# Optimization experiments

Hardware: AMD Instinct MI355X
Metric: run time of the kernel (lower is better)

Reference implementation:

```python
import jax, jax.numpy as jnp
import numpy as np

HIDDEN = 128
RHO = 5        # K // 2 with K = 10
J = 5
SCALE = 5.0


def setup_inputs() -> dict:
    key = jax.random.key(0)
    ks = jax.random.split(key, 16)
    B, N, D = 2, 4096, HIDDEN
    eigvs = jax.random.uniform(ks[0], (B, N, D), dtype=jnp.float32)  # eigenvalue encodings in [0,1)
    x = jax.random.normal(ks[1], (B, N, D), dtype=jnp.float32)
    U = jax.random.normal(ks[2], (B, N, N), dtype=jnp.float32) / np.sqrt(N)
    s = 1.0 / np.sqrt(D)
    return {
        "eigvs": eigvs, "x": x, "U": U,
        # Linear weights stored as [in, out] (already transposed vs torch)
        "Wa": jax.random.normal(ks[3], (D, RHO), dtype=jnp.float32) * s,
        "ba": jnp.zeros((RHO,), jnp.float32),
        "Wb": jax.random.normal(ks[4], (D, RHO), dtype=jnp.float32) * s,
        "bb": jnp.zeros((RHO,), jnp.float32),
        "Ws": jax.random.normal(ks[5], (D, J), dtype=jnp.float32) * s,
        "bs": jnp.zeros((J,), jnp.float32),
        "WS": jax.random.normal(ks[6], (D, D), dtype=jnp.float32) * s,
        "bS": jnp.zeros((D,), jnp.float32),
        "WM": jax.random.normal(ks[7], (J, D, D), dtype=jnp.float32) * s,
        "bM": jnp.zeros((J, D), jnp.float32),
        "Ww": jax.random.normal(ks[8], (D, D), dtype=jnp.float32) * s,
        "bw": jnp.zeros((D,), jnp.float32),
    }


def _generate_g(a, sx, rho):
    # a: [B, rho]; sx: [B, J, N, D] scaled eigenvalues. Even Chebyshev polys.
    T_odd = jnp.ones_like(sx)
    T_even = sx
    g = a[:, 0, None, None, None] * T_even
    for i in range(1, rho):
        T_odd = 2.0 * sx * T_even - T_odd
        T_even = 2.0 * sx * T_odd - T_even
        g = g + a[:, i, None, None, None] * T_even
    return g


def _generate_h(b, e, rho):
    # b: [B, rho]; e: [B, N, D]. Odd Chebyshev polys.
    T_odd = jnp.ones_like(e)
    T_even = e
    h = b[:, 0, None, None] * T_odd
    for i in range(1, rho):
        T_odd = 2.0 * e * T_even - T_odd
        T_even = 2.0 * e * T_odd - T_even
        h = h + b[:, i, None, None] * T_odd
    return h


def reference(eigvs, x, U, Wa, ba, Wb, bb, Ws, bs, WS, bS, WM, bM, Ww, bw):
    # Filter coefficients from pooled eigenvalue encodings
    a_tilde = (eigvs @ Wa + ba).mean(axis=-2)                      # [B, rho]
    b_tilde = (eigvs @ Wb + bb).mean(axis=-2)                      # [B, rho]
    scale_tilde = jax.nn.sigmoid((eigvs @ Ws + bs).mean(axis=-2)) * SCALE  # [B, J]

    h = _generate_h(b_tilde, eigvs, RHO)                           # [B, N, D] scaling filter
    sx = scale_tilde[:, :, None, None] * eigvs[:, None]            # [B, J, N, D]
    g = _generate_g(a_tilde, sx, RHO)                              # [B, J, N, D] wavelet filters

    # Spectral convolution: U diag(filter) U^T x, per channel
    xt = jnp.einsum('bmn,bmd->bnd', U, x)                          # U^T x
    y_h = jnp.einsum('bnm,bmd->bnd', U, h * xt)                    # [B, N, D]
    y_g = jnp.einsum('bnm,bjmd->bjnd', U, g * xt[:, None])         # [B, J, N, D]

    out = y_h @ WS + bS                                            # S_kernel
    out = out + jnp.einsum('bjnd,jde->bne', y_g, WM) + bM.sum(0)   # sum_j M_kernels[j]
    return out @ Ww + bw                                           # W
```

## Files before the change

kernel.cpp:

```cpp
#include <hip/hip_runtime.h>
#include <hip/hip_bf16.h>
#include <stdint.h>

typedef unsigned short u16;
typedef __attribute__((ext_vector_type(8))) short bf16x8;
typedef __attribute__((ext_vector_type(4))) float f32x4;
typedef __attribute__((ext_vector_type(4))) uint32_t u32x4;

__device__ inline u16 f2bf(float f) {
  union { float f; uint32_t u; } v; v.f = f;
  uint32_t u = v.u;
  u += 0x7FFFu + ((u >> 16) & 1u);
  return (u16)(u >> 16);
}
__device__ inline uint32_t pkbf(float a, float b) {
  union { __hip_bfloat162 h; uint32_t u; } c;
  c.h = __float22bfloat162_rn(float2{a, b});
  return c.u;
}
__device__ inline float bf2f(u16 h) {
  union { uint32_t u; float f; } v; v.u = (uint32_t)h << 16; return v.f;
}
__device__ inline void gl_lds16(const void* g, void* s) {
  __builtin_amdgcn_global_load_lds(
      (const __attribute__((address_space(1))) void*)(uintptr_t)(g),
      (__attribute__((address_space(3))) void*)(uint32_t)(uintptr_t)(s),
      16, 0, 0);
}

__global__ __launch_bounds__(256) void k_pre(
    const float* __restrict__ eig, const float* __restrict__ x,
    const float* __restrict__ U,
    const float* __restrict__ WS, const float* __restrict__ WM,
    const float* __restrict__ Ww, const float* __restrict__ bS,
    const float* __restrict__ bM, const float* __restrict__ bw,
    float* __restrict__ part, u16* __restrict__ xT,
    u16* __restrict__ VT, float* __restrict__ cvec,
    u16* __restrict__ Ubf, u16* __restrict__ UTr) {
  const int bid = blockIdx.x, t = threadIdx.x;
  __shared__ float red[256];
  __shared__ uint32_t L[64][33];
  if (bid < 64) {
    const int b = bid >> 5, chunk = bid & 31;
    const int d = t & 127, half = t >> 7;
    const float* p = eig + ((long)b * 4096 + chunk * 128 + half) * 128 + d;
    float s = 0.0f;
    for (int i = 0; i < 64; i++) s += p[(long)i * 256];
    red[t] = s;
    __syncthreads();
    if (t < 128) part[((long)b * 32 + chunk) * 128 + d] = red[t] + red[t + 128];
    return;
  }
  if (bid < 320) {
    const int q = bid - 64;
    const int b = q >> 7, rem = q & 127;
    const int tr = rem & 63, tc = rem >> 6;
    const float* I = x + (long)b * 524288;
    u16* O = xT + (long)b * 524288;
    const int r = t >> 2, cq = (t & 3) * 4;
    const float* src = I + (long)(tr * 64 + r) * 128 + tc * 64;
#pragma unroll
    for (int i = 0; i < 4; i++) {
      const float4 f = *(const float4*)(src + cq + 16 * i);
      const int c = cq + 16 * i;
      L[r][(c >> 1)]     = pkbf(f.x, f.y);
      L[r][(c >> 1) + 1] = pkbf(f.z, f.w);
    }
    __syncthreads();
    const int r0 = (t & 7) * 8;
#pragma unroll
    for (int p = 0; p < 2; p++) {
      const int c = (t >> 3) + 32 * p;
      uint32_t w[4];
#pragma unroll
      for (int i = 0; i < 4; i++) {
        const uint32_t w0 = L[r0 + 2 * i][c >> 1];
        const uint32_t w1 = L[r0 + 2 * i + 1][c >> 1];
        const u16 v0 = (c & 1) ? (u16)(w0 >> 16) : (u16)(w0 & 0xffff);
        const u16 v1 = (c & 1) ? (u16)(w1 >> 16) : (u16)(w1 & 0xffff);
        w[i] = (uint32_t)v0 | ((uint32_t)v1 << 16);
      }
      u32x4* dst = (u32x4*)(O + (long)(tc * 64 + c) * 4096 + tr * 64 + r0);
      *dst = u32x4{w[0], w[1], w[2], w[3]};
    }
    return;
  }
  if (bid < 704) {
    const int q = (bid - 320) * 2 + (t >> 7);
    const int e = t & 127;
    const int f = q >> 7, d = q & 127;
    const float* Frow = (f == 0) ? (WS + d * 128) : (WM + ((long)(f - 1) * 128 + d) * 128);
    float s = 0.0f;
    for (int k = 0; k < 128; k++) s += Frow[k] * Ww[k * 128 + e];
    VT[(long)e * 768 + f * 128 + d] = f2bf(s);
    return;
  }
  if (bid == 704) {
    if (t >= 128) return;
    float s = bw[t];
    for (int k = 0; k < 128; k++) {
      float tv = bS[k];
#pragma unroll
      for (int j = 0; j < 5; j++) tv += bM[j * 128 + k];
      s += tv * Ww[k * 128 + t];
    }
    cvec[t] = s;
    return;
  }
  {
    const int q = bid - 705;
    const int b = q >> 12, rem = q & 4095;
    const int ti = rem & 63, tj = rem >> 6;
    const float* Iu = U + (long)b * 16777216 + (long)ti * 64 * 4096 + tj * 64;
    u16* Ou = Ubf + (long)b * 16777216 + (long)ti * 64 * 4096 + tj * 64;
    u16* Ot = UTr + (long)b * 16777216 + (long)tj * 64 * 4096 + ti * 64;
    const int r = t >> 2, cq = (t & 3) * 4;
    const float* src = Iu + (long)r * 4096 + cq;
    u16* dstS = Ou + (long)r * 4096 + cq;
#pragma unroll
    for (int i = 0; i < 4; i++) {
      const float4 f = *(const float4*)(src + 16 * i);
      const int c = cq + 16 * i;
      *(uint2*)(dstS + 16 * i) = uint2{pkbf(f.x, f.y), pkbf(f.z, f.w)};
      L[r][(c >> 1)]     = pkbf(f.x, f.y);
      L[r][(c >> 1) + 1] = pkbf(f.z, f.w);
    }
    __syncthreads();
    const int r0 = (t & 7) * 8;
#pragma unroll
    for (int p = 0; p < 2; p++) {
      const int c = (t >> 3) + 32 * p;
      uint32_t w[4];
#pragma unroll
      for (int i = 0; i < 4; i++) {
        const uint32_t w0 = L[r0 + 2 * i][c >> 1];
        const uint32_t w1 = L[r0 + 2 * i + 1][c >> 1];
        const u16 v0 = (c & 1) ? (u16)(w0 >> 16) : (u16)(w0 & 0xffff);
        const u16 v1 = (c & 1) ? (u16)(w1 >> 16) : (u16)(w1 & 0xffff);
        w[i] = (uint32_t)v0 | ((uint32_t)v1 << 16);
      }
      u32x4* dst = (u32x4*)(Ot + (long)c * 4096 + r0);
      *dst = u32x4{w[0], w[1], w[2], w[3]};
    }
  }
}


__global__ __launch_bounds__(256) void k_gemm1(
    const u16* __restrict__ xT, const u16* __restrict__ UTr,
    const float* __restrict__ part,
    const float* __restrict__ Wa, const float* __restrict__ ba,
    const float* __restrict__ Wb, const float* __restrict__ bb_,
    const float* __restrict__ Ws, const float* __restrict__ bs,
    float* __restrict__ xs, float* __restrict__ coeff) {
  const int tn = blockIdx.x, ks = blockIdx.y, bb = blockIdx.z;
  const int tid = threadIdx.x;
  __shared__ float sd[128];
  __shared__ __align__(16) u16 As[3 * 4096];
  __shared__ __align__(16) u16 Bs[3 * 4096];
  if (tn == 32) {
    if (ks != 0) return;
    if (tid < 128) {
      float s = 0.0f;
      for (int c = 0; c < 32; c++) s += part[((long)bb * 32 + c) * 128 + tid];
      sd[tid] = s * (1.0f / 4096.0f);
    }
    __syncthreads();
    if (tid >= 15) return;
    const int kind = tid / 5, r = tid % 5;
    const float* W = (kind == 0) ? Wa : ((kind == 1) ? Wb : Ws);
    float v = 0.0f;
    for (int d = 0; d < 128; d++) v += sd[d] * W[d * 5 + r];
    v += (kind == 0) ? ba[r] : ((kind == 1) ? bb_[r] : bs[r]);
    if (kind == 2) v = 5.0f / (1.0f + __expf(-v));
    coeff[bb * 16 + kind * 5 + r] = v;
    return;
  }
  const int wave = tid >> 6, lane = tid & 63;
  const int wm = (wave >> 1) * 64, wn = (wave & 1) * 64;
  f32x4 acc[4][4];
#pragma unroll
  for (int i = 0; i < 4; i++)
#pragma unroll
    for (int j = 0; j < 4; j++)
#pragma unroll
      for (int r = 0; r < 4; r++) acc[i][j][r] = 0.0f;
  const int swz_rd = ((lane >> 4) ^ ((lane >> 1) & 3)) * 16;
  const int a_off = (wm + (lane & 15)) * 64 + swz_rd;
  const int b_off = (wn + (lane & 15)) * 64 + swz_rd;
  const int srow = wave * 32 + (lane >> 2);
  const int scol = ((lane & 3) ^ ((lane >> 3) & 3)) * 8;
  const u16* Asrc = xT + (long)bb * 524288 + ks * 512 + scol;
  const u16* Bsrc = UTr + (long)bb * 16777216 + (long)tn * 524288 + ks * 512 + scol;

  auto STAGE = [&](int k0, int buf) {
    char* dA = (char*)As + buf * 8192 + wave * 2048;
    char* dB = (char*)Bs + buf * 8192 + wave * 2048;
    gl_lds16(Asrc + (long)srow * 4096 + k0, dA);
    gl_lds16(Asrc + (long)(srow + 16) * 4096 + k0, dA + 1024);
    gl_lds16(Bsrc + (long)srow * 4096 + k0, dB);
    gl_lds16(Bsrc + (long)(srow + 16) * 4096 + k0, dB + 1024);
  };
  auto COMPUTE = [&](int buf) {
    bf16x8 af[4], bfr[4];
    const char* Ab_ = (const char*)As + buf * 8192 + a_off;
    const char* Bb_ = (const char*)Bs + buf * 8192 + b_off;
#pragma unroll
    for (int mt = 0; mt < 4; mt++) af[mt] = *(const bf16x8*)(Ab_ + mt * 1024);
#pragma unroll
    for (int nt = 0; nt < 4; nt++) bfr[nt] = *(const bf16x8*)(Bb_ + nt * 1024);
#pragma unroll
    for (int mt = 0; mt < 4; mt++)
#pragma unroll
      for (int nt = 0; nt < 4; nt++)
        acc[mt][nt] = __builtin_amdgcn_mfma_f32_16x16x32_bf16(af[mt], bfr[nt], acc[mt][nt], 0, 0, 0);
  };

  STAGE(0, 0);
  STAGE(32, 1);
  asm volatile("s_waitcnt vmcnt(4)" ::: "memory");
  __builtin_amdgcn_s_barrier();
  __builtin_amdgcn_sched_barrier(0);
#pragma unroll
  for (int t = 0; t < 14; ++t) {
    STAGE((t + 2) * 32, (t + 2) % 3);
    COMPUTE(t % 3);
    asm volatile("s_waitcnt vmcnt(4)" ::: "memory");
    __builtin_amdgcn_s_barrier();
    __builtin_amdgcn_sched_barrier(0);
  }
  COMPUTE(2);
  asm volatile("s_waitcnt vmcnt(0)" ::: "memory");
  __builtin_amdgcn_s_barrier();
  __builtin_amdgcn_sched_barrier(0);
  COMPUTE(0);

  const int lr = (lane >> 4) * 4, lc = lane & 15;
  float* Cf = xs + (long)bb * 524288 + (long)ks * 1048576;
#pragma unroll
  for (int mt = 0; mt < 4; mt++)
#pragma unroll
    for (int nt = 0; nt < 4; nt++) {
      const int col = tn * 128 + wn + nt * 16 + lc;
#pragma unroll
      for (int r = 0; r < 4; r++) {
        const int row = wm + mt * 16 + lr + r;
        Cf[(long)col * 128 + row] = acc[mt][nt][r];
      }
    }
}

__global__ void k_filter(const float* __restrict__ eig, const float* __restrict__ xs,
                         const float* __restrict__ coeff, u16* __restrict__ Mod) {
  const int b = blockIdx.y;
  const int n = blockIdx.x * 2 + (threadIdx.x >> 7);
  const int d = threadIdx.x & 127;
  const long ridx = (long)b * 4096 + n;
  const long off = ridx * 128 + d;
  const float e = eig[off];
  float xv = 0.0f;
#pragma unroll
  for (int s = 0; s < 8; s++) xv += xs[off + (long)s * 1048576];
  const float* cf = coeff + b * 16;
  float To = 1.0f, Tev = e;
  float h = cf[5];
#pragma unroll
  for (int i = 1; i < 5; i++) {
    To = 2.0f * e * Tev - To;
    Tev = 2.0f * e * To - Tev;
    h += cf[5 + i] * To;
  }
  u16* row = Mod + ridx * 768;
  row[d] = f2bf(h * xv);
#pragma unroll
  for (int j = 0; j < 5; j++) {
    const float sx = cf[10 + j] * e;
    float To2 = 1.0f, Te2 = sx;
    float g = cf[0] * Te2;
#pragma unroll
    for (int i = 1; i < 5; i++) {
      To2 = 2.0f * sx * Te2 - To2;
      Te2 = 2.0f * sx * To2 - Te2;
      g += cf[i] * Te2;
    }
    row[(j + 1) * 128 + d] = f2bf(g * xv);
  }
}

__global__ __launch_bounds__(256) void k_gemm2(
    const u16* __restrict__ VT, const u16* __restrict__ Mod, u16* __restrict__ wT) {
  const int tn = blockIdx.x, bb = blockIdx.z;
  __shared__ __align__(16) u16 As[3 * 4096];
  __shared__ __align__(16) u16 Bs[3 * 4096];
  const int tid = threadIdx.x, wave = tid >> 6, lane = tid & 63;
  const int wm = (wave >> 1) * 64, wn = (wave & 1) * 64;
  f32x4 acc[4][4];
#pragma unroll
  for (int i = 0; i < 4; i++)
#pragma unroll
    for (int j = 0; j < 4; j++)
#pragma unroll
      for (int r = 0; r < 4; r++) acc[i][j][r] = 0.0f;
  const int swz_rd = ((lane >> 4) ^ ((lane >> 1) & 3)) * 16;
  const int a_off = (wm + (lane & 15)) * 64 + swz_rd;
  const int b_off = (wn + (lane & 15)) * 64 + swz_rd;
  const int srow = wave * 32 + (lane >> 2);
  const int scol = ((lane & 3) ^ ((lane >> 3) & 3)) * 8;
  const u16* Asrc = VT + scol;
  const u16* Bsrc = Mod + (long)bb * 3145728 + (long)tn * 98304 + scol;

  auto STAGE = [&](int k0, int buf) {
    char* dA = (char*)As + buf * 8192 + wave * 2048;
    char* dB = (char*)Bs + buf * 8192 + wave * 2048;
    gl_lds16(Asrc + (long)srow * 768 + k0, dA);
    gl_lds16(Asrc + (long)(srow + 16) * 768 + k0, dA + 1024);
    gl_lds16(Bsrc + (long)srow * 768 + k0, dB);
    gl_lds16(Bsrc + (long)(srow + 16) * 768 + k0, dB + 1024);
  };
  auto COMPUTE = [&](int buf) {
    bf16x8 af[4], bfr[4];
    const char* Ab_ = (const char*)As + buf * 8192 + a_off;
    const char* Bb_ = (const char*)Bs + buf * 8192 + b_off;
#pragma unroll
    for (int mt = 0; mt < 4; mt++) af[mt] = *(const bf16x8*)(Ab_ + mt * 1024);
#pragma unroll
    for (int nt = 0; nt < 4; nt++) bfr[nt] = *(const bf16x8*)(Bb_ + nt * 1024);
#pragma unroll
    for (int mt = 0; mt < 4; mt++)
#pragma unroll
      for (int nt = 0; nt < 4; nt++)
        acc[mt][nt] = __builtin_amdgcn_mfma_f32_16x16x32_bf16(af[mt], bfr[nt], acc[mt][nt], 0, 0, 0);
  };

  STAGE(0, 0);
  STAGE(32, 1);
  asm volatile("s_waitcnt vmcnt(4)" ::: "memory");
  __builtin_amdgcn_s_barrier();
  __builtin_amdgcn_sched_barrier(0);
#pragma unroll
  for (int t = 0; t < 22; ++t) {
    STAGE((t + 2) * 32, (t + 2) % 3);
    COMPUTE(t % 3);
    asm volatile("s_waitcnt vmcnt(4)" ::: "memory");
    __builtin_amdgcn_s_barrier();
    __builtin_amdgcn_sched_barrier(0);
  }
  COMPUTE(1);
  asm volatile("s_waitcnt vmcnt(0)" ::: "memory");
  __builtin_amdgcn_s_barrier();
  __builtin_amdgcn_sched_barrier(0);
  COMPUTE(2);

  const int lr = (lane >> 4) * 4, lc = lane & 15;
  u16* Cb = wT + (long)bb * 524288;
#pragma unroll
  for (int mt = 0; mt < 4; mt++)
#pragma unroll
    for (int nt = 0; nt < 4; nt++) {
      const int col = tn * 128 + wn + nt * 16 + lc;
#pragma unroll
      for (int r = 0; r < 4; r++) {
        const int row = wm + mt * 16 + lr + r;
        Cb[(long)row * 4096 + col] = f2bf(acc[mt][nt][r]);
      }
    }
}

__global__ __launch_bounds__(256) void k_gemm3(
    const u16* __restrict__ Ubf, const u16* __restrict__ wT, u16* __restrict__ os16) {
  const int tm = blockIdx.x, ks = blockIdx.y, bb = blockIdx.z;
  __shared__ __align__(16) u16 As[3 * 4096];
  __shared__ __align__(16) u16 Bs[3 * 4096];
  const int tid = threadIdx.x, wave = tid >> 6, lane = tid & 63;
  const int wm = (wave >> 1) * 64, wn = (wave & 1) * 64;
  f32x4 acc[4][4];
#pragma unroll
  for (int i = 0; i < 4; i++)
#pragma unroll
    for (int j = 0; j < 4; j++)
#pragma unroll
      for (int r = 0; r < 4; r++) acc[i][j][r] = 0.0f;
  const int swz_rd = ((lane >> 4) ^ ((lane >> 1) & 3)) * 16;
  const int a_off = (wm + (lane & 15)) * 64 + swz_rd;
  const int b_off = (wn + (lane & 15)) * 64 + swz_rd;
  const int srow = wave * 32 + (lane >> 2);
  const int scol = ((lane & 3) ^ ((lane >> 3) & 3)) * 8;
  const u16* Asrc = Ubf + (long)bb * 16777216 + (long)tm * 524288 + ks * 512 + scol;
  const u16* Bsrc = wT + (long)bb * 524288 + ks * 512 + scol;

  auto STAGE = [&](int k0, int buf) {
    char* dA = (char*)As + buf * 8192 + wave * 2048;
    char* dB = (char*)Bs + buf * 8192 + wave * 2048;
    gl_lds16(Asrc + (long)srow * 4096 + k0, dA);
    gl_lds16(Asrc + (long)(srow + 16) * 4096 + k0, dA + 1024);
    gl_lds16(Bsrc + (long)srow * 4096 + k0, dB);
    gl_lds16(Bsrc + (long)(srow + 16) * 4096 + k0, dB + 1024);
  };
  auto COMPUTE = [&](int buf) {
    bf16x8 af[4], bfr[4];
    const char* Ab_ = (const char*)As + buf * 8192 + a_off;
    const char* Bb_ = (const char*)Bs + buf * 8192 + b_off;
#pragma unroll
    for (int mt = 0; mt < 4; mt++) af[mt] = *(const bf16x8*)(Ab_ + mt * 1024);
#pragma unroll
    for (int nt = 0; nt < 4; nt++) bfr[nt] = *(const bf16x8*)(Bb_ + nt * 1024);
#pragma unroll
    for (int mt = 0; mt < 4; mt++)
#pragma unroll
      for (int nt = 0; nt < 4; nt++)
        acc[mt][nt] = __builtin_amdgcn_mfma_f32_16x16x32_bf16(af[mt], bfr[nt], acc[mt][nt], 0, 0, 0);
  };

  STAGE(0, 0);
  STAGE(32, 1);
  asm volatile("s_waitcnt vmcnt(4)" ::: "memory");
  __builtin_amdgcn_s_barrier();
  __builtin_amdgcn_sched_barrier(0);
#pragma unroll
  for (int t = 0; t < 14; ++t) {
    STAGE((t + 2) * 32, (t + 2) % 3);
    COMPUTE(t % 3);
    asm volatile("s_waitcnt vmcnt(4)" ::: "memory");
    __builtin_amdgcn_s_barrier();
    __builtin_amdgcn_sched_barrier(0);
  }
  COMPUTE(2);
  asm volatile("s_waitcnt vmcnt(0)" ::: "memory");
  __builtin_amdgcn_s_barrier();
  __builtin_amdgcn_sched_barrier(0);
  COMPUTE(0);

  const int lr = (lane >> 4) * 4, lc = lane & 15;
  u16* Cb = os16 + (long)ks * 1048576 + (long)bb * 524288;
#pragma unroll
  for (int mt = 0; mt < 4; mt++)
#pragma unroll
    for (int nt = 0; nt < 4; nt++) {
      const int col = wn + nt * 16 + lc;
#pragma unroll
      for (int r = 0; r < 4; r++) {
        const int row = tm * 128 + wm + mt * 16 + lr + r;
        Cb[(long)row * 128 + col] = f2bf(acc[mt][nt][r]);
      }
    }
}

__global__ void k_outred(const u16* __restrict__ os16, const float* __restrict__ cvec,
                         float* __restrict__ out) {
  const long i = (long)blockIdx.x * 256 + threadIdx.x;
  const long j4 = i * 4;
  float4 r = {0.0f, 0.0f, 0.0f, 0.0f};
#pragma unroll
  for (int s = 0; s < 8; s++) {
    const uint2 v = *(const uint2*)(os16 + j4 + (long)s * 1048576);
    r.x += bf2f((u16)(v.x & 0xffff));
    r.y += bf2f((u16)(v.x >> 16));
    r.z += bf2f((u16)(v.y & 0xffff));
    r.w += bf2f((u16)(v.y >> 16));
  }
  const float4 cv = *(const float4*)(cvec + (i & 31) * 4);
  r.x += cv.x; r.y += cv.y; r.z += cv.z; r.w += cv.w;
  *(float4*)(out + j4) = r;
}

extern "C" void kernel_launch(void* const* d_in, const int* in_sizes, int n_in,
                              void* d_out, int out_size, void* d_ws, size_t ws_size,
                              hipStream_t stream) {
  const float* eig = (const float*)d_in[0];
  const float* x   = (const float*)d_in[1];
  const float* U   = (const float*)d_in[2];
  const float* Wa  = (const float*)d_in[3];
  const float* ba  = (const float*)d_in[4];
  const float* Wb  = (const float*)d_in[5];
  const float* bb  = (const float*)d_in[6];
  const float* Ws  = (const float*)d_in[7];
  const float* bs  = (const float*)d_in[8];
  const float* WSm = (const float*)d_in[9];
  const float* bS  = (const float*)d_in[10];
  const float* WM  = (const float*)d_in[11];
  const float* bM  = (const float*)d_in[12];
  const float* Ww  = (const float*)d_in[13];
  const float* bw  = (const float*)d_in[14];

  char* ws = (char*)d_ws;
  float* xs   = (float*)(ws + 0);
  u16*   os16 = (u16*)(ws + 0);
  u16*   Mod  = (u16*)(ws + 33554432);
  u16*   xT   = (u16*)(ws + 46137344);
  u16*   wT   = (u16*)(ws + 48234496);
  u16*   VT   = (u16*)(ws + 50331648);
  float* part = (float*)(ws + 50528256);
  float* coef = (float*)(ws + 50561024);
  float* cvec = (float*)(ws + 50561152);
  u16*   Ubf  = (u16*)(ws + 52428800);
  u16*   UTr  = (u16*)(ws + 119537664);
  float* outp = (float*)d_out;

  if (ws_size < (size_t)186646528) return;

  k_pre<<<8897, 256, 0, stream>>>(eig, x, U, WSm, WM, Ww, bS, bM, bw,
                                  part, xT, VT, cvec, Ubf, UTr);

  k_gemm1<<<dim3(33, 8, 2), 256, 0, stream>>>(xT, UTr, part, Wa, ba, Wb, bb, Ws, bs, xs, coef);

  k_filter<<<dim3(2048, 2), 256, 0, stream>>>(eig, xs, coef, Mod);

  k_gemm2<<<dim3(32, 1, 2), 256, 0, stream>>>(VT, Mod, wT);

  k_gemm3<<<dim3(32, 8, 2), 256, 0, stream>>>(Ubf, wT, os16);

  k_outred<<<1024, 256, 0, stream>>>(os16, cvec, outp);
}
```

Measured before the change: 329.3 us.

## Use 128x128 tiles for U conversion/transpose and deepen GEMM pipelines to four stages

```diff
diff --git a/kernel.cpp b/kernel.cpp
--- a/kernel.cpp
+++ b/kernel.cpp
@@ -38,17 +38,20 @@
     u16* __restrict__ VT, float* __restrict__ cvec,
     u16* __restrict__ Ubf, u16* __restrict__ UTr) {
   const int bid = blockIdx.x, t = threadIdx.x;
-  __shared__ float red[256];
-  __shared__ uint32_t L[64][33];
+  __shared__ union {
+    float red[256];
+    uint32_t L[64][33];
+    uint32_t Lp[128 * 72];
+  } sh;
   if (bid < 64) {
     const int b = bid >> 5, chunk = bid & 31;
     const int d = t & 127, half = t >> 7;
     const float* p = eig + ((long)b * 4096 + chunk * 128 + half) * 128 + d;
     float s = 0.0f;
     for (int i = 0; i < 64; i++) s += p[(long)i * 256];
-    red[t] = s;
+    sh.red[t] = s;
     __syncthreads();
-    if (t < 128) part[((long)b * 32 + chunk) * 128 + d] = red[t] + red[t + 128];
+    if (t < 128) part[((long)b * 32 + chunk) * 128 + d] = sh.red[t] + sh.red[t + 128];
     return;
   }
   if (bid < 320) {
@@ -63,8 +66,8 @@
     for (int i = 0; i < 4; i++) {
       const float4 f = *(const float4*)(src + cq + 16 * i);
       const int c = cq + 16 * i;
-      L[r][(c >> 1)]     = pkbf(f.x, f.y);
-      L[r][(c >> 1) + 1] = pkbf(f.z, f.w);
+      sh.L[r][(c >> 1)]     = pkbf(f.x, f.y);
+      sh.L[r][(c >> 1) + 1] = pkbf(f.z, f.w);
     }
     __syncthreads();
     const int r0 = (t & 7) * 8;
@@ -74,8 +77,8 @@
       uint32_t w[4];
 #pragma unroll
       for (int i = 0; i < 4; i++) {
-        const uint32_t w0 = L[r0 + 2 * i][c >> 1];
-        const uint32_t w1 = L[r0 + 2 * i + 1][c >> 1];
+        const uint32_t w0 = sh.L[r0 + 2 * i][c >> 1];
+        const uint32_t w1 = sh.L[r0 + 2 * i + 1][c >> 1];
         const u16 v0 = (c & 1) ? (u16)(w0 >> 16) : (u16)(w0 & 0xffff);
         const u16 v1 = (c & 1) ? (u16)(w1 >> 16) : (u16)(w1 & 0xffff);
         w[i] = (uint32_t)v0 | ((uint32_t)v1 << 16);
@@ -109,38 +112,49 @@
   }
   {
     const int q = bid - 705;
-    const int b = q >> 12, rem = q & 4095;
-    const int ti = rem & 63, tj = rem >> 6;
-    const float* Iu = U + (long)b * 16777216 + (long)ti * 64 * 4096 + tj * 64;
-    u16* Ou = Ubf + (long)b * 16777216 + (long)ti * 64 * 4096 + tj * 64;
-    u16* Ot = UTr + (long)b * 16777216 + (long)tj * 64 * 4096 + ti * 64;
-    const int r = t >> 2, cq = (t & 3) * 4;
-    const float* src = Iu + (long)r * 4096 + cq;
-    u16* dstS = Ou + (long)r * 4096 + cq;
+    const int b = q >> 10;
+    const int rem = q & 1023;
+    const int ti = rem & 31;
+    const int tj = rem >> 5;
+    const long ubase = (long)b * 16777216 + (long)(ti * 128) * 4096 + tj * 128;
+    const float* Iu = U + ubase;
+    u16* Os = Ubf + ubase;
+    u16* Ot = UTr + (long)b * 16777216 + (long)(tj * 128) * 4096 + ti * 128;
+    const int a = t >> 2;
+    const int c0 = (t & 3) * 32;
+    const float* r0 = Iu + (long)(2 * a) * 4096 + c0;
+    const float* r1 = r0 + 4096;
+    float4 f0[8], f1[8];
+#pragma unroll
+    for (int i = 0; i < 8; i++) {
+      f0[i] = *(const float4*)(r0 + 4 * i);
+      f1[i] = *(const float4*)(r1 + 4 * i);
+    }
+    u16* d0 = Os + (long)(2 * a) * 4096 + c0;
+    u16* d1 = d0 + 4096;
 #pragma unroll
     for (int i = 0; i < 4; i++) {
-      const float4 f = *(const float4*)(src + 16 * i);
-      const int c = cq + 16 * i;
-      *(uint2*)(dstS + 16 * i) = uint2{pkbf(f.x, f.y), pkbf(f.z, f.w)};
-      L[r][(c >> 1)]     = pkbf(f.x, f.y);
-      L[r][(c >> 1) + 1] = pkbf(f.z, f.w);
+      *(u32x4*)(d0 + 8 * i) = u32x4{pkbf(f0[2*i].x, f0[2*i].y), pkbf(f0[2*i].z, f0[2*i].w),
+                                    pkbf(f0[2*i+1].x, f0[2*i+1].y), pkbf(f0[2*i+1].z, f0[2*i+1].w)};
+      *(u32x4*)(d1 + 8 * i) = u32x4{pkbf(f1[2*i].x, f1[2*i].y), pkbf(f1[2*i].z, f1[2*i].w),
+                                    pkbf(f1[2*i+1].x, f1[2*i+1].y), pkbf(f1[2*i+1].z, f1[2*i+1].w)};
+    }
+#pragma unroll
+    for (int i = 0; i < 8; i++) {
+      const int n = c0 + 4 * i;
+      sh.Lp[(n + 0) * 72 + a] = pkbf(f0[i].x, f1[i].x);
+      sh.Lp[(n + 1) * 72 + a] = pkbf(f0[i].y, f1[i].y);
+      sh.Lp[(n + 2) * 72 + a] = pkbf(f0[i].z, f1[i].z);
+      sh.Lp[(n + 3) * 72 + a] = pkbf(f0[i].w, f1[i].w);
     }
     __syncthreads();
-    const int r0 = (t & 7) * 8;
-#pragma unroll
-    for (int p = 0; p < 2; p++) {
-      const int c = (t >> 3) + 32 * p;
-      uint32_t w[4];
-#pragma unroll
-      for (int i = 0; i < 4; i++) {
-        const uint32_t w0 = L[r0 + 2 * i][c >> 1];
-        const uint32_t w1 = L[r0 + 2 * i + 1][c >> 1];
-        const u16 v0 = (c & 1) ? (u16)(w0 >> 16) : (u16)(w0 & 0xffff);
-        const u16 v1 = (c & 1) ? (u16)(w1 >> 16) : (u16)(w1 & 0xffff);
-        w[i] = (uint32_t)v0 | ((uint32_t)v1 << 16);
-      }
-      u32x4* dst = (u32x4*)(Ot + (long)c * 4096 + r0);
-      *dst = u32x4{w[0], w[1], w[2], w[3]};
+    const int g = t >> 4;
+    const int j = t & 15;
+#pragma unroll
+    for (int p = 0; p < 8; p++) {
+      const int n = p * 16 + g;
+      const u32x4 v = *(const u32x4*)&sh.Lp[n * 72 + j * 4];
+      *(u32x4*)(Ot + (long)n * 4096 + j * 8) = v;
     }
   }
 }
@@ -156,8 +170,8 @@
   const int tn = blockIdx.x, ks = blockIdx.y, bb = blockIdx.z;
   const int tid = threadIdx.x;
   __shared__ float sd[128];
-  __shared__ __align__(16) u16 As[3 * 4096];
-  __shared__ __align__(16) u16 Bs[3 * 4096];
+  __shared__ __align__(16) u16 As[4 * 4096];
+  __shared__ __align__(16) u16 Bs[4 * 4096];
   if (tn == 32) {
     if (ks != 0) return;
     if (tid < 128) {
@@ -218,22 +232,27 @@
 
   STAGE(0, 0);
   STAGE(32, 1);
-  asm volatile("s_waitcnt vmcnt(4)" ::: "memory");
-  __builtin_amdgcn_s_barrier();
-  __builtin_amdgcn_sched_barrier(0);
-#pragma unroll
-  for (int t = 0; t < 14; ++t) {
-    STAGE((t + 2) * 32, (t + 2) % 3);
-    COMPUTE(t % 3);
-    asm volatile("s_waitcnt vmcnt(4)" ::: "memory");
+  STAGE(64, 2);
+  asm volatile("s_waitcnt vmcnt(8)" ::: "memory");
+  __builtin_amdgcn_s_barrier();
+  __builtin_amdgcn_sched_barrier(0);
+#pragma unroll
+  for (int t = 0; t < 13; ++t) {
+    STAGE((t + 3) * 32, (t + 3) & 3);
+    COMPUTE(t & 3);
+    asm volatile("s_waitcnt vmcnt(8)" ::: "memory");
     __builtin_amdgcn_s_barrier();
     __builtin_amdgcn_sched_barrier(0);
   }
+  COMPUTE(1);
+  asm volatile("s_waitcnt vmcnt(4)" ::: "memory");
+  __builtin_amdgcn_s_barrier();
+  __builtin_amdgcn_sched_barrier(0);
   COMPUTE(2);
   asm volatile("s_waitcnt vmcnt(0)" ::: "memory");
   __builtin_amdgcn_s_barrier();
   __builtin_amdgcn_sched_barrier(0);
-  COMPUTE(0);
+  COMPUTE(3);
 
   const int lr = (lane >> 4) * 4, lc = lane & 15;
   float* Cf = xs + (long)bb * 524288 + (long)ks * 1048576;
@@ -290,8 +309,8 @@
 __global__ __launch_bounds__(256) void k_gemm2(
     const u16* __restrict__ VT, const u16* __restrict__ Mod, u16* __restrict__ wT) {
   const int tn = blockIdx.x, bb = blockIdx.z;
-  __shared__ __align__(16) u16 As[3 * 4096];
-  __shared__ __align__(16) u16 Bs[3 * 4096];
+  __shared__ __align__(16) u16 As[4 * 4096];
+  __shared__ __align__(16) u16 Bs[4 * 4096];
   const int tid = threadIdx.x, wave = tid >> 6, lane = tid & 63;
   const int wm = (wave >> 1) * 64, wn = (wave & 1) * 64;
   f32x4 acc[4][4];
@@ -334,22 +353,27 @@
 
   STAGE(0, 0);
   STAGE(32, 1);
-  asm volatile("s_waitcnt vmcnt(4)" ::: "memory");
-  __builtin_amdgcn_s_barrier();
-  __builtin_amdgcn_sched_barrier(0);
-#pragma unroll
-  for (int t = 0; t < 22; ++t) {
-    STAGE((t + 2) * 32, (t + 2) % 3);
-    COMPUTE(t % 3);
-    asm volatile("s_waitcnt vmcnt(4)" ::: "memory");
+  STAGE(64, 2);
+  asm volatile("s_waitcnt vmcnt(8)" ::: "memory");
+  __builtin_amdgcn_s_barrier();
+  __builtin_amdgcn_sched_barrier(0);
+#pragma unroll
+  for (int t = 0; t < 21; ++t) {
+    STAGE((t + 3) * 32, (t + 3) & 3);
+    COMPUTE(t & 3);
+    asm volatile("s_waitcnt vmcnt(8)" ::: "memory");
     __builtin_amdgcn_s_barrier();
     __builtin_amdgcn_sched_barrier(0);
   }
   COMPUTE(1);
+  asm volatile("s_waitcnt vmcnt(4)" ::: "memory");
+  __builtin_amdgcn_s_barrier();
+  __builtin_amdgcn_sched_barrier(0);
+  COMPUTE(2);
   asm volatile("s_waitcnt vmcnt(0)" ::: "memory");
   __builtin_amdgcn_s_barrier();
   __builtin_amdgcn_sched_barrier(0);
-  COMPUTE(2);
+  COMPUTE(3);
 
   const int lr = (lane >> 4) * 4, lc = lane & 15;
   u16* Cb = wT + (long)bb * 524288;
@@ -369,8 +393,8 @@
 __global__ __launch_bounds__(256) void k_gemm3(
     const u16* __restrict__ Ubf, const u16* __restrict__ wT, u16* __restrict__ os16) {
   const int tm = blockIdx.x, ks = blockIdx.y, bb = blockIdx.z;
-  __shared__ __align__(16) u16 As[3 * 4096];
-  __shared__ __align__(16) u16 Bs[3 * 4096];
+  __shared__ __align__(16) u16 As[4 * 4096];
+  __shared__ __align__(16) u16 Bs[4 * 4096];
   const int tid = threadIdx.x, wave = tid >> 6, lane = tid & 63;
   const int wm = (wave >> 1) * 64, wn = (wave & 1) * 64;
   f32x4 acc[4][4];
@@ -413,22 +437,27 @@
 
   STAGE(0, 0);
   STAGE(32, 1);
-  asm volatile("s_waitcnt vmcnt(4)" ::: "memory");
-  __builtin_amdgcn_s_barrier();
-  __builtin_amdgcn_sched_barrier(0);
-#pragma unroll
-  for (int t = 0; t < 14; ++t) {
-    STAGE((t + 2) * 32, (t + 2) % 3);
-    COMPUTE(t % 3);
-    asm volatile("s_waitcnt vmcnt(4)" ::: "memory");
+  STAGE(64, 2);
+  asm volatile("s_waitcnt vmcnt(8)" ::: "memory");
+  __builtin_amdgcn_s_barrier();
+  __builtin_amdgcn_sched_barrier(0);
+#pragma unroll
+  for (int t = 0; t < 13; ++t) {
+    STAGE((t + 3) * 32, (t + 3) & 3);
+    COMPUTE(t & 3);
+    asm volatile("s_waitcnt vmcnt(8)" ::: "memory");
     __builtin_amdgcn_s_barrier();
     __builtin_amdgcn_sched_barrier(0);
   }
+  COMPUTE(1);
+  asm volatile("s_waitcnt vmcnt(4)" ::: "memory");
+  __builtin_amdgcn_s_barrier();
+  __builtin_amdgcn_sched_barrier(0);
   COMPUTE(2);
   asm volatile("s_waitcnt vmcnt(0)" ::: "memory");
   __builtin_amdgcn_s_barrier();
   __builtin_amdgcn_sched_barrier(0);
-  COMPUTE(0);
+  COMPUTE(3);
 
   const int lr = (lane >> 4) * 4, lc = lane & 15;
   u16* Cb = os16 + (long)ks * 1048576 + (long)bb * 524288;
@@ -498,7 +527,7 @@
 
   if (ws_size < (size_t)186646528) return;
 
-  k_pre<<<8897, 256, 0, stream>>>(eig, x, U, WSm, WM, Ww, bS, bM, bw,
+  k_pre<<<2753, 256, 0, stream>>>(eig, x, U, WSm, WM, Ww, bS, bM, bw,
                                   part, xT, VT, cvec, Ubf, UTr);
 
   k_gemm1<<<dim3(33, 8, 2), 256, 0, stream>>>(xT, UTr, part, Wa, ba, Wb, bb, Ws, bs, xs, coef);
```

New measurement: 333.6 us. No clear change (+1.3%).
